# Optimization experiments

Measured on AMD Instinct MI355X. Metric: run time of the kernel, lower is better.

## Reference

```python
import jax, jax.numpy as jnp
import numpy as np

N_NODES = 10000
N_EDGES = 320000
N_PAIRS = 2048
IN_CH = 128
HIDDEN = 512
OUT_CH = 1

def setup_inputs() -> dict:
    key = jax.random.key(0)
    k = jax.random.split(key, 8)
    x = jax.random.normal(k[0], (N_NODES, IN_CH), dtype=jnp.float32)
    edge_index = jax.random.randint(k[1], (2, N_EDGES), 0, N_NODES, dtype=jnp.int64)
    tar_ei = jax.random.randint(k[2], (2, N_PAIRS), 0, N_NODES, dtype=jnp.int64)
    s1 = 1.0 / np.sqrt(2 * IN_CH)
    s2 = 1.0 / np.sqrt(HIDDEN)
    W1 = jax.random.uniform(k[3], (2 * IN_CH, HIDDEN), jnp.float32, -s1, s1)
    b1 = jax.random.uniform(k[4], (HIDDEN,), jnp.float32, -s1, s1)
    W2 = jax.random.uniform(k[5], (HIDDEN, OUT_CH), jnp.float32, -s2, s2)
    b2 = jax.random.uniform(k[6], (OUT_CH,), jnp.float32, -s2, s2)
    return {"x": x, "edge_index": edge_index, "tar_ei": tar_ei,
            "W1": W1, "b1": b1, "W2": W2, "b2": b2}

def reference(x, edge_index, tar_ei, W1, b1, W2, b2):
    N = x.shape[0]
    # Symmetrized adjacency; coalesce() sums duplicate entries -> scatter-add of ones.
    src = jnp.concatenate([edge_index[0], edge_index[1]])
    dst = jnp.concatenate([edge_index[1], edge_index[0]])
    A = jnp.zeros((N, N), dtype=x.dtype).at[src, dst].add(1.0)  # [N, N]
    ti, tj = tar_ei[0], tar_ei[1]
    Ai = A[ti]  # [B, N] neighbor rows of source endpoints
    Aj = A[tj]  # [B, N] neighbor rows of target endpoints
    # cn_1_1 = Ai * Aj (sparse Hadamard intersection); spmm_add(cn_1_1, x):
    cn_emb = jnp.einsum('bn,bn,nd->bd', Ai, Aj, x)  # [B, in_ch]
    xij = x[ti] * x[tj]                               # [B, in_ch]
    xs = jnp.concatenate([xij, cn_emb], axis=-1)      # [B, 2*in_ch]
    # NOTE: original calls xs.relu() (non in-place) -> no-op, faithfully omitted.
    h = jax.nn.relu(xs @ W1 + b1)
    return h @ W2 + b2
```

## Files before the change

kernel.cpp:

```cpp
#include <hip/hip_runtime.h>

#define N_NODES 10000
#define N_EDGES 320000
#define N_PAIRS 2048
#define IN_CH 128
#define HIDDEN 512
#define PPB 8
#define WIDTH 160
#define NSLOT 4096


__global__ void k_map(const int* __restrict__ tar, int* __restrict__ slotmap,
                      int* __restrict__ cnt) {
    int t = blockIdx.x * blockDim.x + threadIdx.x;
    if (t >= NSLOT) return;
    cnt[t] = 0;
    int v = tar[t];
    atomicCAS(&slotmap[v], -1, t);
}

__global__ void k_edges(const int* __restrict__ ei,
                        const int* __restrict__ slotmap,
                        int* __restrict__ cnt,
                        unsigned short* __restrict__ adjC) {
    int e = blockIdx.x * blockDim.x + threadIdx.x;
    if (e >= N_EDGES) return;
    int s = ei[e];
    int d = ei[N_EDGES + e];
    int sl = slotmap[s];
    if (sl >= 0) {
        int p = atomicAdd(&cnt[sl], 1);
        if (p < WIDTH) adjC[sl * WIDTH + p] = (unsigned short)d;
    }
    sl = slotmap[d];
    if (sl >= 0) {
        int p = atomicAdd(&cnt[sl], 1);
        if (p < WIDTH) adjC[sl * WIDTH + p] = (unsigned short)s;
    }
}

__global__ __launch_bounds__(64) void k_inter(
    const float* __restrict__ x,
    const int* __restrict__ tar,
    const int* __restrict__ slotmap,
    const int* __restrict__ cnt,
    const unsigned short* __restrict__ adjC,
    float* __restrict__ xs) {
    __shared__ unsigned short adjJ[WIDTH];
    const int b = blockIdx.x;
    const int t = threadIdx.x;
    const int ti = tar[b];
    const int tj = tar[N_PAIRS + b];
    const int si = slotmap[ti];
    const int sj = slotmap[tj];
    int cj = cnt[sj]; cj = cj < WIDTH ? cj : WIDTH;
    int ci = cnt[si]; ci = ci < WIDTH ? ci : WIDTH;
    for (int q = t; q < cj; q += 64) adjJ[q] = adjC[sj * WIDTH + q];
    __syncthreads();

    float c0 = 0.0f, c1 = 0.0f;
    const int cir = (ci + 63) & ~63;
    for (int pp = t; pp < cir; pp += 64) {
        const int u = (pp < ci) ? (int)adjC[si * WIDTH + pp] : 0xFFFF;
        int cm = 0;
        for (int q = 0; q < cj; ++q) cm += ((int)adjJ[q] == u) ? 1 : 0;
        unsigned long long m = __ballot(cm > 0);
        while (m) {
            const int lane = __ffsll(m) - 1;
            m &= m - 1;
            const int uu = __shfl(u, lane, 64);
            const float fc = (float)__shfl(cm, lane, 64);
            c0 += fc * x[uu * IN_CH + t];
            c1 += fc * x[uu * IN_CH + 64 + t];
        }
    }

    const float xi0 = x[ti * IN_CH + t], xi1 = x[ti * IN_CH + 64 + t];
    const float xj0 = x[tj * IN_CH + t], xj1 = x[tj * IN_CH + 64 + t];
    float* __restrict__ row = xs + (size_t)b * (2 * IN_CH);
    row[t]       = xi0 * xj0;
    row[64 + t]  = xi1 * xj1;
    row[128 + t] = c0;
    row[192 + t] = c1;
}

__global__ __launch_bounds__(256) void k_mlp(
    const float* __restrict__ xs,
    const float* __restrict__ W1,
    const float* __restrict__ b1,
    const float* __restrict__ W2,
    const float* __restrict__ b2,
    float* __restrict__ out) {
    __shared__ float sxs[PPB][2 * IN_CH];
    __shared__ float red[PPB][4];
    const int tid = threadIdx.x;
    const int base = blockIdx.x * PPB;
#pragma unroll
    for (int r = 0; r < PPB; ++r) sxs[r][tid] = xs[(size_t)(base + r) * 256 + tid];
    const float bja = b1[tid], bjb = b1[tid + 256];
    const float w2a = W2[tid], w2b = W2[tid + 256];
    __syncthreads();

    float acc0[PPB], acc1[PPB];
#pragma unroll
    for (int p = 0; p < PPB; ++p) { acc0[p] = 0.0f; acc1[p] = 0.0f; }
#pragma unroll 8
    for (int k = 0; k < 2 * IN_CH; ++k) {
        const float wa = W1[k * HIDDEN + tid];
        const float wb = W1[k * HIDDEN + tid + 256];
#pragma unroll
        for (int p = 0; p < PPB; ++p) {
            acc0[p] = fmaf(sxs[p][k], wa, acc0[p]);
            acc1[p] = fmaf(sxs[p][k], wb, acc1[p]);
        }
    }

    const int lane = tid & 63;
    const int wid = tid >> 6;
#pragma unroll
    for (int p = 0; p < PPB; ++p) {
        float ha = acc0[p] + bja; ha = ha > 0.0f ? ha : 0.0f;
        float hb = acc1[p] + bjb; hb = hb > 0.0f ? hb : 0.0f;
        float part = ha * w2a + hb * w2b;
        for (int off = 32; off >= 1; off >>= 1)
            part += __shfl_down(part, off, 64);
        if (lane == 0) red[p][wid] = part;
    }
    __syncthreads();
    if (tid < PPB) {
        out[base + tid] = b2[0] + red[tid][0] + red[tid][1] + red[tid][2] + red[tid][3];
    }
}

extern "C" void kernel_launch(void* const* d_in, const int* in_sizes, int n_in,
                              void* d_out, int out_size, void* d_ws, size_t ws_size,
                              hipStream_t stream) {
    const float* x   = (const float*)d_in[0];
    const int*   ei  = (const int*)d_in[1];
    const int*   tar = (const int*)d_in[2];
    const float* W1  = (const float*)d_in[3];
    const float* b1  = (const float*)d_in[4];
    const float* W2  = (const float*)d_in[5];
    const float* b2  = (const float*)d_in[6];
    float* out = (float*)d_out;

    int* ws = (int*)d_ws;
    int* slotmap          = ws;
    int* cnt              = ws + 10240;
    unsigned short* adjC  = (unsigned short*)(ws + 14336);
    float* xs             = (float*)(ws + 342016);

    hipMemsetAsync(slotmap, 0xFF, 10240 * sizeof(int), stream);
    k_map<<<NSLOT / 256, 256, 0, stream>>>(tar, slotmap, cnt);
    k_edges<<<(N_EDGES + 255) / 256, 256, 0, stream>>>(ei, slotmap, cnt, adjC);
    k_inter<<<N_PAIRS, 64, 0, stream>>>(x, tar, slotmap, cnt, adjC, xs);
    k_mlp<<<N_PAIRS / PPB, 256, 0, stream>>>(xs, W1, b1, W2, b2, out);
}
```

Measured before the change: 119.7 us.

## Fuse edge scan, intersection and MLP into one persistent kernel with grid barrier

```diff
diff --git a/kernel.cpp b/kernel.cpp
--- a/kernel.cpp
+++ b/kernel.cpp
@@ -8,99 +8,102 @@
 #define PPB 8
 #define WIDTH 160
 #define NSLOT 4096
+#define NBLK 256
+#define NTHR 256
 
 
-__global__ void k_map(const int* __restrict__ tar, int* __restrict__ slotmap,
-                      int* __restrict__ cnt) {
-    int t = blockIdx.x * blockDim.x + threadIdx.x;
-    if (t >= NSLOT) return;
-    cnt[t] = 0;
-    int v = tar[t];
-    atomicCAS(&slotmap[v], -1, t);
+__global__ __launch_bounds__(1024) void k_init(const int* __restrict__ tar,
+                                               int* __restrict__ ws) {
+    const int t = threadIdx.x;
+    for (int i = t; i < 14344; i += 1024) ws[i] = (i < 10240) ? -1 : 0;
+    __syncthreads();
+    for (int s = t; s < 2 * N_PAIRS; s += 1024) ws[tar[s]] = s;
 }
 
-__global__ void k_edges(const int* __restrict__ ei,
-                        const int* __restrict__ slotmap,
-                        int* __restrict__ cnt,
-                        unsigned short* __restrict__ adjC) {
-    int e = blockIdx.x * blockDim.x + threadIdx.x;
-    if (e >= N_EDGES) return;
-    int s = ei[e];
-    int d = ei[N_EDGES + e];
-    int sl = slotmap[s];
-    if (sl >= 0) {
-        int p = atomicAdd(&cnt[sl], 1);
-        if (p < WIDTH) adjC[sl * WIDTH + p] = (unsigned short)d;
-    }
-    sl = slotmap[d];
-    if (sl >= 0) {
-        int p = atomicAdd(&cnt[sl], 1);
-        if (p < WIDTH) adjC[sl * WIDTH + p] = (unsigned short)s;
-    }
-}
-
-__global__ __launch_bounds__(64) void k_inter(
+__global__ __launch_bounds__(NTHR, 4) void k_mega(
     const float* __restrict__ x,
+    const int* __restrict__ ei,
     const int* __restrict__ tar,
-    const int* __restrict__ slotmap,
-    const int* __restrict__ cnt,
-    const unsigned short* __restrict__ adjC,
-    float* __restrict__ xs) {
-    __shared__ unsigned short adjJ[WIDTH];
-    const int b = blockIdx.x;
-    const int t = threadIdx.x;
-    const int ti = tar[b];
-    const int tj = tar[N_PAIRS + b];
-    const int si = slotmap[ti];
-    const int sj = slotmap[tj];
-    int cj = cnt[sj]; cj = cj < WIDTH ? cj : WIDTH;
-    int ci = cnt[si]; ci = ci < WIDTH ? ci : WIDTH;
-    for (int q = t; q < cj; q += 64) adjJ[q] = adjC[sj * WIDTH + q];
-    __syncthreads();
-
-    float c0 = 0.0f, c1 = 0.0f;
-    const int cir = (ci + 63) & ~63;
-    for (int pp = t; pp < cir; pp += 64) {
-        const int u = (pp < ci) ? (int)adjC[si * WIDTH + pp] : 0xFFFF;
-        int cm = 0;
-        for (int q = 0; q < cj; ++q) cm += ((int)adjJ[q] == u) ? 1 : 0;
-        unsigned long long m = __ballot(cm > 0);
-        while (m) {
-            const int lane = __ffsll(m) - 1;
-            m &= m - 1;
-            const int uu = __shfl(u, lane, 64);
-            const float fc = (float)__shfl(cm, lane, 64);
-            c0 += fc * x[uu * IN_CH + t];
-            c1 += fc * x[uu * IN_CH + 64 + t];
-        }
-    }
-
-    const float xi0 = x[ti * IN_CH + t], xi1 = x[ti * IN_CH + 64 + t];
-    const float xj0 = x[tj * IN_CH + t], xj1 = x[tj * IN_CH + 64 + t];
-    float* __restrict__ row = xs + (size_t)b * (2 * IN_CH);
-    row[t]       = xi0 * xj0;
-    row[64 + t]  = xi1 * xj1;
-    row[128 + t] = c0;
-    row[192 + t] = c1;
-}
-
-__global__ __launch_bounds__(256) void k_mlp(
-    const float* __restrict__ xs,
     const float* __restrict__ W1,
     const float* __restrict__ b1,
     const float* __restrict__ W2,
     const float* __restrict__ b2,
-    float* __restrict__ out) {
+    float* __restrict__ out,
+    int* __restrict__ ws) {
+    int* slotmap = ws;
+    int* cnt = ws + 10240;
+    int* bar = ws + 14336;
+    unsigned short* adjC = (unsigned short*)(ws + 14400);
+
+    const int tid = threadIdx.x;
+    __shared__ unsigned short adjJ[PPB][WIDTH];
     __shared__ float sxs[PPB][2 * IN_CH];
     __shared__ float red[PPB][4];
-    const int tid = threadIdx.x;
-    const int base = blockIdx.x * PPB;
-#pragma unroll
-    for (int r = 0; r < PPB; ++r) sxs[r][tid] = xs[(size_t)(base + r) * 256 + tid];
+
+    for (int e = blockIdx.x * NTHR + tid; e < N_EDGES; e += NBLK * NTHR) {
+        const int s = ei[e];
+        const int d = ei[N_EDGES + e];
+        int sl = slotmap[s];
+        if (sl >= 0) {
+            const int p = atomicAdd(&cnt[sl], 1);
+            if (p < WIDTH) adjC[sl * WIDTH + p] = (unsigned short)d;
+        }
+        sl = slotmap[d];
+        if (sl >= 0) {
+            const int p = atomicAdd(&cnt[sl], 1);
+            if (p < WIDTH) adjC[sl * WIDTH + p] = (unsigned short)s;
+        }
+    }
+
+    __syncthreads();
+    if (tid == 0) {
+        __threadfence();
+        __hip_atomic_fetch_add(&bar[0], 1, __ATOMIC_ACQ_REL, __HIP_MEMORY_SCOPE_AGENT);
+        while (__hip_atomic_load(&bar[0], __ATOMIC_ACQUIRE, __HIP_MEMORY_SCOPE_AGENT) < NBLK)
+            __builtin_amdgcn_s_sleep(2);
+        __threadfence();
+    }
+    __syncthreads();
+
+    {
+        const int wid = tid >> 6;
+        const int lane = tid & 63;
+        for (int pi = 0; pi < 2; ++pi) {
+            const int p = wid + pi * 4;
+            const int pr = blockIdx.x * PPB + p;
+            const int ti = tar[pr];
+            const int tj = tar[N_PAIRS + pr];
+            const int si = slotmap[ti];
+            const int sj = slotmap[tj];
+            int cj = cnt[sj]; cj = cj < WIDTH ? cj : WIDTH;
+            int ci = cnt[si]; ci = ci < WIDTH ? ci : WIDTH;
+            for (int q = lane; q < cj; q += 64) adjJ[p][q] = adjC[sj * WIDTH + q];
+            float c0 = 0.0f, c1 = 0.0f;
+            const int cir = (ci + 63) & ~63;
+            for (int pp = lane; pp < cir; pp += 64) {
+                const int u = (pp < ci) ? (int)adjC[si * WIDTH + pp] : 0x7FFFFFFF;
+                int cm = 0;
+                for (int q = 0; q < cj; ++q) cm += ((int)adjJ[p][q] == u) ? 1 : 0;
+                unsigned long long m = __ballot(cm > 0);
+                while (m) {
+                    const int l2 = __ffsll(m) - 1;
+                    m &= m - 1;
+                    const int uu = __shfl(u, l2, 64);
+                    const float fc = (float)__shfl(cm, l2, 64);
+                    c0 += fc * x[uu * IN_CH + lane];
+                    c1 += fc * x[uu * IN_CH + 64 + lane];
+                }
+            }
+            sxs[p][128 + lane] = c0;
+            sxs[p][192 + lane] = c1;
+            sxs[p][lane]      = x[ti * IN_CH + lane] * x[tj * IN_CH + lane];
+            sxs[p][64 + lane] = x[ti * IN_CH + 64 + lane] * x[tj * IN_CH + 64 + lane];
+        }
+    }
+    __syncthreads();
+
     const float bja = b1[tid], bjb = b1[tid + 256];
     const float w2a = W2[tid], w2b = W2[tid + 256];
-    __syncthreads();
-
     float acc0[PPB], acc1[PPB];
 #pragma unroll
     for (int p = 0; p < PPB; ++p) { acc0[p] = 0.0f; acc1[p] = 0.0f; }
@@ -114,7 +117,6 @@
             acc1[p] = fmaf(sxs[p][k], wb, acc1[p]);
         }
     }
-
     const int lane = tid & 63;
     const int wid = tid >> 6;
 #pragma unroll
@@ -128,7 +130,8 @@
     }
     __syncthreads();
     if (tid < PPB) {
-        out[base + tid] = b2[0] + red[tid][0] + red[tid][1] + red[tid][2] + red[tid][3];
+        out[blockIdx.x * PPB + tid] =
+            b2[0] + red[tid][0] + red[tid][1] + red[tid][2] + red[tid][3];
     }
 }
 
@@ -143,16 +146,8 @@
     const float* W2  = (const float*)d_in[5];
     const float* b2  = (const float*)d_in[6];
     float* out = (float*)d_out;
+    int* ws = (int*)d_ws;
 
-    int* ws = (int*)d_ws;
-    int* slotmap          = ws;
-    int* cnt              = ws + 10240;
-    unsigned short* adjC  = (unsigned short*)(ws + 14336);
-    float* xs             = (float*)(ws + 342016);
-
-    hipMemsetAsync(slotmap, 0xFF, 10240 * sizeof(int), stream);
-    k_map<<<NSLOT / 256, 256, 0, stream>>>(tar, slotmap, cnt);
-    k_edges<<<(N_EDGES + 255) / 256, 256, 0, stream>>>(ei, slotmap, cnt, adjC);
-    k_inter<<<N_PAIRS, 64, 0, stream>>>(x, tar, slotmap, cnt, adjC, xs);
-    k_mlp<<<N_PAIRS / PPB, 256, 0, stream>>>(xs, W1, b1, W2, b2, out);
+    k_init<<<1, 1024, 0, stream>>>(tar, ws);
+    k_mega<<<NBLK, NTHR, 0, stream>>>(x, ei, tar, W1, b1, W2, b2, out, ws);
 }
```

New measurement: 163.7 us. 1.37x slower.
